# Kernel tuning notes

Measured on AMD Instinct MI355X. Metric: run time of the kernel, lower is better.

## Reference

```python
import jax, jax.numpy as jnp
import numpy as np

B, S, D = 2, 2048, 4096
H, KV, HD = 32, 8, 128          # query heads, kv heads, head_dim
N_REP = H // KV                 # GQA groups = 4
ROPE_THETA = 1000000.0


def setup_inputs() -> dict:
    key = jax.random.key(0)
    ks = jax.random.split(key, 8)
    s = 0.02
    return {
        "hidden_states": jax.random.normal(ks[0], (B, S, D), jnp.float32),
        "position_ids": jnp.broadcast_to(jnp.arange(S, dtype=jnp.int32)[None, :], (B, S)),
        "wq": jax.random.normal(ks[1], (D, H * HD), jnp.float32) * s,
        "bq": jax.random.normal(ks[2], (H * HD,), jnp.float32) * s,
        "wk": jax.random.normal(ks[3], (D, KV * HD), jnp.float32) * s,
        "bk": jax.random.normal(ks[4], (KV * HD,), jnp.float32) * s,
        "wv": jax.random.normal(ks[5], (D, KV * HD), jnp.float32) * s,
        "bv": jax.random.normal(ks[6], (KV * HD,), jnp.float32) * s,
        "wo": jax.random.normal(ks[7], (H * HD, D), jnp.float32) * s,
    }


def _rope_cos_sin(position_ids, head_dim, theta):
    pos = position_ids.astype(jnp.float32)
    dim = head_dim // 2
    freqs = 1.0 / theta ** (jnp.arange(0, dim, dtype=jnp.float32) / dim)
    t = pos[..., None] * freqs[None, None, :]          # [B,S,dim]
    return jnp.cos(t)[..., None, :], jnp.sin(t)[..., None, :]  # [B,S,1,dim]


def _apply_rope(x, cos, sin):
    half = x.shape[-1] // 2
    x1, x2 = x[..., :half], x[..., half:]
    return jnp.concatenate([x1 * cos - x2 * sin, x1 * sin + x2 * cos], axis=-1)


def reference(hidden_states, position_ids, wq, bq, wk, bk, wv, bv, wo):
    q = (hidden_states @ wq + bq).reshape(B, S, H, HD)
    k = (hidden_states @ wk + bk).reshape(B, S, KV, HD)
    v = (hidden_states @ wv + bv).reshape(B, S, KV, HD)

    cos, sin = _rope_cos_sin(position_ids, HD, ROPE_THETA)
    q = _apply_rope(q, cos, sin)
    k = _apply_rope(k, cos, sin)

    # GQA: physically expand KV heads (adjacent repeats, matches repeat_kv)
    k = jnp.repeat(k, N_REP, axis=2)   # [B,S,H,HD]
    v = jnp.repeat(v, N_REP, axis=2)

    # causal bias (attention_mask defaults to all-ones, so only causal matters)
    neg = jnp.finfo(jnp.float32).min
    causal = jnp.tril(jnp.ones((S, S), dtype=bool))
    bias = jnp.where(causal, 0.0, neg).astype(jnp.float32)  # [S,S]

    scale = 1.0 / jnp.sqrt(jnp.float32(HD))
    scores = jnp.einsum("bqhd,bkhd->bhqk", q * scale, k) + bias[None, None]
    attn = jax.nn.softmax(scores, axis=-1)                  # [B,H,S,S]
    out = jnp.einsum("bhqk,bkhd->bqhd", attn, v)
    out = out.reshape(B, S, H * HD)
    return out @ wo
```

## Files before the change

kernel.cpp:

```cpp
#include <hip/hip_runtime.h>
#include <hip/hip_bf16.h>
#include <math.h>


typedef __bf16 bf16;
typedef __attribute__((ext_vector_type(8))) __bf16 bf16x8;
typedef __attribute__((ext_vector_type(4))) float f32x4;

__device__ __forceinline__ void glds16(const void* g, void* l) {
    __builtin_amdgcn_global_load_lds(
        (const __attribute__((address_space(1))) void*)g,
        (__attribute__((address_space(3))) void*)l, 16, 0, 0);
}

__device__ __forceinline__ unsigned cvt_pk_bf16(float lo, float hi) {
    unsigned r;
    asm("v_cvt_pk_bf16_f32 %0, %1, %2" : "=v"(r) : "v"(lo), "v"(hi));
    return r;
}

__global__ __launch_bounds__(256) void convert_kernel(
    const float* __restrict__ in, bf16* __restrict__ out)
{
    const size_t i0 = ((size_t)blockIdx.x * 256 + threadIdx.x) * 8;
    const float4 a = *(const float4*)(in + i0);
    const float4 b = *(const float4*)(in + i0 + 4);
    bf16x8 p;
    p[0] = (bf16)a.x; p[1] = (bf16)a.y; p[2] = (bf16)a.z; p[3] = (bf16)a.w;
    p[4] = (bf16)b.x; p[5] = (bf16)b.y; p[6] = (bf16)b.z; p[7] = (bf16)b.w;
    *(bf16x8*)(out + i0) = p;
}

__global__ __launch_bounds__(256) void transpose_conv_kernel(
    const float* __restrict__ in, bf16* __restrict__ out, int N)
{
    __shared__ bf16 tile[32 * 68];
    const int n0 = blockIdx.x * 32, k0 = blockIdx.y * 64;
    const int t = threadIdx.x;
    const int nn = t & 31, kk0 = (t >> 5) * 8;
#pragma unroll
    for (int j = 0; j < 8; ++j)
        tile[nn * 68 + kk0 + j] = (bf16)in[(size_t)(k0 + kk0 + j) * N + n0 + nn];
    __syncthreads();
    const int n2 = t >> 3, c = (t & 7) * 8;
    *(bf16x8*)(out + (size_t)(n0 + n2) * 4096 + k0 + c) = *(const bf16x8*)(&tile[n2 * 68 + c]);
}

#define G256_LDA(dst, bufv, mh)                                                 \
    do {                                                                        \
        _Pragma("unroll")                                                       \
        for (int m_ = 0; m_ < 4; ++m_) {                                        \
            const int rowh_ = (m_ * 2 + wr) * 16 + l15;                         \
            const int colp_ = (quad * 8) ^ (((rowh_ >> 3) & 1) << 4);           \
            const int bse_ = ((bufv) * 2 + (mh)) * 8192 + rowh_ * 32 + colp_;   \
            dst[m_][0] = *(const bf16x8*)&Lds[bse_];                            \
            dst[m_][1] = *(const bf16x8*)&Lds[bse_ + 4096];                     \
        }                                                                       \
    } while (0)

#define G256_LDB(dst, bufv, nh)                                                 \
    do {                                                                        \
        _Pragma("unroll")                                                       \
        for (int n_ = 0; n_ < 2; ++n_) {                                        \
            const int rowh_ = (n_ * 4 + wc) * 16 + l15;                         \
            const int colp_ = (quad * 8) ^ (((rowh_ >> 3) & 1) << 4);           \
            const int bse_ = 32768 + ((bufv) * 2 + (nh)) * 8192 +               \
                             rowh_ * 32 + colp_;                                \
            dst[n_][0] = *(const bf16x8*)&Lds[bse_];                            \
            dst[n_][1] = *(const bf16x8*)&Lds[bse_ + 4096];                     \
        }                                                                       \
    } while (0)

#define G256_QUAD(av, bv, mh, nh)                                               \
    do {                                                                        \
        __builtin_amdgcn_s_setprio(1);                                          \
        _Pragma("unroll")                                                       \
        for (int m_ = 0; m_ < 4; ++m_)                                          \
            _Pragma("unroll")                                                   \
            for (int n_ = 0; n_ < 2; ++n_) {                                    \
                acc[(mh) * 4 + m_][(nh) * 2 + n_] =                             \
                    __builtin_amdgcn_mfma_f32_16x16x32_bf16(                    \
                        av[m_][0], bv[n_][0], acc[(mh) * 4 + m_][(nh) * 2 + n_],\
                        0, 0, 0);                                               \
                acc[(mh) * 4 + m_][(nh) * 2 + n_] =                             \
                    __builtin_amdgcn_mfma_f32_16x16x32_bf16(                    \
                        av[m_][1], bv[n_][1], acc[(mh) * 4 + m_][(nh) * 2 + n_],\
                        0, 0, 0);                                               \
            }                                                                   \
        __builtin_amdgcn_s_setprio(0);                                          \
    } while (0)

template <int EPI>
__global__ __launch_bounds__(512) void gemm256_kernel(
    const bf16* __restrict__ A,
    const bf16* __restrict__ BqT, const bf16* __restrict__ BkT, const bf16* __restrict__ BvT,
    const float* __restrict__ b_q, const float* __restrict__ b_k, const float* __restrict__ b_v,
    bf16* __restrict__ q_out, bf16* __restrict__ kv_k, bf16* __restrict__ kv_v,
    float* __restrict__ f_out, int nwg)
{
    __shared__ bf16 Lds[65536];

    const int tid = threadIdx.x;
    const int wv = tid >> 6, lane = tid & 63;
    const int l15 = lane & 15, quad = lane >> 4;
    const int wr = wv >> 2, wc = wv & 3;

    const int bid = blockIdx.x;
    const int swz = (bid & 7) * (nwg >> 3) + (bid >> 3);
    const int mt = swz & 15, nt = swz >> 4;
    const int row0 = mt * 256;

    const bf16* BT;
    const float* biasp = nullptr;
    bf16* dstkv = nullptr;
    int sel = 0, bcol0, ocol0 = nt * 256, lcol0 = 0;
    if (EPI == 0) {
        if (nt < 16)      { BT = BqT; bcol0 = nt * 256; biasp = b_q + nt * 256; sel = 0; }
        else if (nt < 20) { BT = BkT; bcol0 = (nt - 16) * 256; biasp = b_k + (nt - 16) * 256;
                            sel = 1; dstkv = kv_k; lcol0 = (nt - 16) * 256; }
        else              { BT = BvT; bcol0 = (nt - 20) * 256; biasp = b_v + (nt - 20) * 256;
                            sel = 2; dstkv = kv_v; lcol0 = (nt - 20) * 256; }
    } else {
        BT = BqT; bcol0 = nt * 256;
    }

    auto stage = [&](int n) {
        if (n >= 256) return;
        const int T = n >> 2, j = n & 3;
        const int buf = T & 1;
        const bool isA = (j == 0 || j == 3);
        const int half = (j == 0) ? 0 : (j == 3) ? 1 : (j - 1);
        const int k0 = T * 64;
        const bf16* g = isA ? (A + (size_t)(row0 + half * 128) * 4096)
                            : (BT + (size_t)(bcol0 + half * 128) * 4096);
        bf16* lb = &Lds[(isA ? 0 : 32768) + (buf * 2 + half) * 8192];
#pragma unroll
        for (int jj = 0; jj < 2; ++jj) {
            const int pc = (wv * 2 + jj) * 64 + lane;
            const int kk = pc >> 9, rem = pc & 511;
            const int row = rem >> 2, ccp = rem & 3;
            const int ccl = ccp ^ ((row >> 2) & 2);
            glds16(g + (size_t)row * 4096 + k0 + kk * 32 + ccl * 8,
                   lb + (wv * 2 + jj) * 512);
        }
    };

    const f32x4 vzero = {0.f, 0.f, 0.f, 0.f};
    f32x4 acc[8][4];
#pragma unroll
    for (int mi = 0; mi < 8; ++mi)
#pragma unroll
        for (int ni = 0; ni < 4; ++ni) acc[mi][ni] = vzero;

    bf16x8 a[4][2], b0[2][2], b1[2][2];

    for (int n = 0; n < 7; ++n) stage(n);
    asm volatile("s_waitcnt vmcnt(6)" ::: "memory");
    __builtin_amdgcn_s_barrier();

    for (int t = 0; t < 64; ++t) {
        const int buf = t & 1;
        const int nb = 4 * t;
        G256_LDA(a, buf, 0);
        G256_LDB(b0, buf, 0);
        stage(nb + 7);
        __builtin_amdgcn_s_barrier();
        G256_QUAD(a, b0, 0, 0);
        __builtin_amdgcn_s_barrier();
        G256_LDB(b1, buf, 1);
        stage(nb + 8);
        __builtin_amdgcn_s_barrier();
        G256_QUAD(a, b1, 0, 1);
        __builtin_amdgcn_s_barrier();
        G256_LDA(a, buf, 1);
        stage(nb + 9);
        __builtin_amdgcn_s_barrier();
        G256_QUAD(a, b0, 1, 0);
        __builtin_amdgcn_s_barrier();
        stage(nb + 10);
        __builtin_amdgcn_s_barrier();
        G256_QUAD(a, b1, 1, 1);
        if (t < 62)       asm volatile("s_waitcnt vmcnt(6)" ::: "memory");
        else if (t == 62) asm volatile("s_waitcnt vmcnt(0)" ::: "memory");
        __builtin_amdgcn_s_barrier();
    }

#pragma unroll
    for (int mi = 0; mi < 8; ++mi) {
        const int mtile = (mi >> 2) * 8 + (mi & 3) * 2 + wr;
#pragma unroll
        for (int ni = 0; ni < 4; ++ni) {
            const int ntile = ni * 4 + wc;
            const int gcl = ntile * 16 + l15;
#pragma unroll
            for (int i = 0; i < 4; ++i) {
                const int gr = row0 + mtile * 16 + quad * 4 + i;
                float vv = acc[mi][ni][i];
                if (EPI == 1) {
                    f_out[(size_t)gr * 4096 + ocol0 + gcl] = vv;
                } else {
                    vv += biasp[gcl];
                    if (sel == 0) {
                        q_out[(size_t)gr * 4096 + ocol0 + gcl] = (bf16)vv;
                    } else {
                        const int lc = lcol0 + gcl;
                        dstkv[(size_t)((gr >> 11) * 8 + (lc >> 7)) * 262144 +
                              (size_t)(gr & 2047) * 128 + (lc & 127)] = (bf16)vv;
                    }
                }
            }
        }
    }
}

template <int EPI, int AF32>
__global__ __launch_bounds__(256) void gemm_kernel(
    const float* __restrict__ A_f32, const bf16* __restrict__ A_bf16,
    const bf16* __restrict__ BqT, const bf16* __restrict__ BkT, const bf16* __restrict__ BvT,
    const float* __restrict__ b_q, const float* __restrict__ b_k, const float* __restrict__ b_v,
    bf16* __restrict__ q_out, bf16* __restrict__ kv_k, bf16* __restrict__ kv_v,
    float* __restrict__ f_out)
{
    constexpr int LDA = AF32 ? 34 : 32;
    __shared__ bf16 As[128 * LDA];
    __shared__ bf16 Bs[128 * 32];

    const int nt = blockIdx.x, mt = blockIdx.y;
    const int tid = threadIdx.x;
    const int wave = tid >> 6, lane = tid & 63;
    const int l15 = lane & 15, quad = lane >> 4;
    const int wm = (wave >> 1) * 64, wn = (wave & 1) * 64;

    const bf16* BT;
    const float* bias = nullptr;
    int sel = 0, ncol0;
    if (EPI == 0) {
        if (nt < 32)      { BT = BqT; bias = b_q; sel = 0; ncol0 = nt * 128; }
        else if (nt < 40) { BT = BkT; bias = b_k; sel = 1; ncol0 = (nt - 32) * 128; }
        else              { BT = BvT; bias = b_v; sel = 2; ncol0 = (nt - 40) * 128; }
    } else {
        BT = BqT; ncol0 = nt * 128;
    }
    const int row0 = mt * 128;

    const f32x4 vzero = {0.f, 0.f, 0.f, 0.f};
    f32x4 acc[4][4];
#pragma unroll
    for (int mi = 0; mi < 4; ++mi)
#pragma unroll
        for (int ni = 0; ni < 4; ++ni) acc[mi][ni] = vzero;

    const int a_row = tid >> 1, a_seg = (tid & 1) * 16;
    const int g_row = lane >> 2, g_seg = (lane & 3) * 8;

    for (int k0 = 0; k0 < 4096; k0 += 32) {
        if (AF32) {
            const float4* src = (const float4*)(A_f32 + (size_t)(row0 + a_row) * 4096 + k0 + a_seg);
            float4 f0 = src[0], f1 = src[1], f2 = src[2], f3 = src[3];
            bf16x8 p0, p1;
            p0[0] = (bf16)f0.x; p0[1] = (bf16)f0.y; p0[2] = (bf16)f0.z; p0[3] = (bf16)f0.w;
            p0[4] = (bf16)f1.x; p0[5] = (bf16)f1.y; p0[6] = (bf16)f1.z; p0[7] = (bf16)f1.w;
            p1[0] = (bf16)f2.x; p1[1] = (bf16)f2.y; p1[2] = (bf16)f2.z; p1[3] = (bf16)f2.w;
            p1[4] = (bf16)f3.x; p1[5] = (bf16)f3.y; p1[6] = (bf16)f3.z; p1[7] = (bf16)f3.w;
            *(bf16x8*)(&As[a_row * LDA + a_seg]) = p0;
            *(bf16x8*)(&As[a_row * LDA + a_seg + 8]) = p1;
        } else {
#pragma unroll
            for (int c = 0; c < 2; ++c)
                glds16(A_bf16 + (size_t)(row0 + wave * 32 + c * 16 + g_row) * 4096 + k0 + g_seg,
                       &As[(wave * 32 + c * 16) * 32]);
        }
#pragma unroll
        for (int c = 0; c < 2; ++c)
            glds16(BT + (size_t)(ncol0 + wave * 32 + c * 16 + g_row) * 4096 + k0 + g_seg,
                   &Bs[(wave * 32 + c * 16) * 32]);
        __syncthreads();

        bf16x8 af[4], bfv[4];
#pragma unroll
        for (int mi = 0; mi < 4; ++mi)
            af[mi] = *(const bf16x8*)(&As[(wm + mi * 16 + l15) * LDA + quad * 8]);
#pragma unroll
        for (int ni = 0; ni < 4; ++ni)
            bfv[ni] = *(const bf16x8*)(&Bs[(wn + ni * 16 + l15) * 32 + quad * 8]);
#pragma unroll
        for (int mi = 0; mi < 4; ++mi)
#pragma unroll
            for (int ni = 0; ni < 4; ++ni)
                acc[mi][ni] = __builtin_amdgcn_mfma_f32_16x16x32_bf16(af[mi], bfv[ni], acc[mi][ni], 0, 0, 0);
        __syncthreads();
    }

#pragma unroll
    for (int mi = 0; mi < 4; ++mi)
#pragma unroll
        for (int ni = 0; ni < 4; ++ni)
#pragma unroll
            for (int i = 0; i < 4; ++i) {
                const int gr = row0 + wm + mi * 16 + quad * 4 + i;
                const int gc = ncol0 + wn + ni * 16 + l15;
                float vv = acc[mi][ni][i];
                if (EPI == 1) {
                    f_out[(size_t)gr * 4096 + gc] = vv;
                } else {
                    vv += bias[gc];
                    if (sel == 0) {
                        q_out[(size_t)gr * 4096 + gc] = (bf16)vv;
                    } else {
                        bf16* dst = (sel == 1) ? kv_k : kv_v;
                        dst[(size_t)((gr >> 11) * 8 + (gc >> 7)) * 262144 +
                            (size_t)(gr & 2047) * 128 + (gc & 127)] = (bf16)vv;
                    }
                }
            }
}

__global__ __launch_bounds__(256) void rope_q_kernel(
    bf16* __restrict__ q, const int* __restrict__ pos_ids)
{
    const int idx = blockIdx.x * 256 + threadIdx.x;
    const int d = idx & 63, h = (idx >> 6) & 31, tok = idx >> 11;
    const float posv = (float)pos_ids[tok];
    const float fr = exp2f((float)d * (-19.931568569324174f / 64.f));
    float sn, cs;
    sincosf(posv * fr, &sn, &cs);
    bf16* xp = q + (size_t)tok * 4096 + h * 128 + d;
    const float x1 = (float)xp[0], x2 = (float)xp[64];
    const float scale = 0.08838834764831845f;
    xp[0]  = (bf16)((x1 * cs - x2 * sn) * scale);
    xp[64] = (bf16)((x1 * sn + x2 * cs) * scale);
}

__global__ __launch_bounds__(256) void rope_k_kernel(
    bf16* __restrict__ k, const int* __restrict__ pos_ids)
{
    const int idx = blockIdx.x * 256 + threadIdx.x;
    const int d = idx & 63, s = (idx >> 6) & 2047, bk = idx >> 17;
    const int b = bk >> 3;
    const float posv = (float)pos_ids[b * 2048 + s];
    const float fr = exp2f((float)d * (-19.931568569324174f / 64.f));
    float sn, cs;
    sincosf(posv * fr, &sn, &cs);
    bf16* xp = k + ((size_t)bk * 2048 + s) * 128 + d;
    const float x1 = (float)xp[0], x2 = (float)xp[64];
    xp[0]  = (bf16)(x1 * cs - x2 * sn);
    xp[64] = (bf16)(x1 * sn + x2 * cs);
}

__global__ __launch_bounds__(256) void attn_kernel(
    const bf16* __restrict__ q, const bf16* __restrict__ k,
    const bf16* __restrict__ v, bf16* __restrict__ o)
{
    __shared__ bf16 Ksl[64 * 136];
    __shared__ bf16 Vsl[128 * 72];
    __shared__ bf16 Psl[4 * 16 * 68];

    const int pair = blockIdx.x & 7;
    const int h  = (blockIdx.x >> 3) & 31;
    const int b  = blockIdx.x >> 8;
    const int kvh = h >> 2;
    const int tid = threadIdx.x;
    const int wave = tid >> 6, lane = tid & 63;
    const int l15 = lane & 15, quad = lane >> 4;

    const bf16* kbase = k + (size_t)(b * 8 + kvh) * 2048 * 128;
    const bf16* vbase = v + (size_t)(b * 8 + kvh) * 2048 * 128;

    const int kr = tid >> 2, ksg = (tid & 3) * 32;
    const f32x4 vzero = {0.f, 0.f, 0.f, 0.f};

#pragma unroll 1
    for (int phase = 0; phase < 2; ++phase) {
        const int qt = phase ? (15 - pair) : pair;
        const int qbase = qt * 128 + wave * 32;

        bf16x8 qf[2][4];
#pragma unroll
        for (int mi = 0; mi < 2; ++mi) {
            const bf16* qrow = q + ((size_t)(b * 2048 + qbase + mi * 16 + l15) * 32 + h) * 128;
#pragma unroll
            for (int kb = 0; kb < 4; ++kb)
                qf[mi][kb] = *(const bf16x8*)(qrow + kb * 32 + quad * 8);
        }

        f32x4 acc_o[2][8];
#pragma unroll
        for (int mi = 0; mi < 2; ++mi)
#pragma unroll
            for (int i = 0; i < 8; ++i) acc_o[mi][i] = vzero;
        float m_i[2] = {-INFINITY, -INFINITY};
        float l_i[2] = {0.f, 0.f};

        const int nT = 2 * qt + 2;
        for (int t = 0; t < nT; ++t) {
            const int kv0 = t * 64;
            {
                const bf16x8* ks = (const bf16x8*)(kbase + (size_t)(kv0 + kr) * 128 + ksg);
                bf16x8* kd = (bf16x8*)(&Ksl[kr * 136 + ksg]);
                kd[0] = ks[0]; kd[1] = ks[1]; kd[2] = ks[2]; kd[3] = ks[3];
            }
            {
                const bf16x8* vs = (const bf16x8*)(vbase + (size_t)(kv0 + lane) * 128 + wave * 32);
                bf16x8 w0 = vs[0], w1 = vs[1], w2 = vs[2], w3 = vs[3];
#pragma unroll
                for (int i = 0; i < 8; ++i) {
                    Vsl[(wave * 32 + i)      * 72 + lane] = w0[i];
                    Vsl[(wave * 32 + 8 + i)  * 72 + lane] = w1[i];
                    Vsl[(wave * 32 + 16 + i) * 72 + lane] = w2[i];
                    Vsl[(wave * 32 + 24 + i) * 72 + lane] = w3[i];
                }
            }
            __syncthreads();

            if (kv0 <= qbase + 31) {
                f32x4 sacc[2][4];
#pragma unroll
                for (int mi = 0; mi < 2; ++mi)
#pragma unroll
                    for (int nt = 0; nt < 4; ++nt) sacc[mi][nt] = vzero;
                __builtin_amdgcn_s_setprio(1);
#pragma unroll
                for (int nt = 0; nt < 4; ++nt)
#pragma unroll
                    for (int kb = 0; kb < 4; ++kb) {
                        const bf16x8 kf = *(const bf16x8*)(&Ksl[(nt * 16 + l15) * 136 + kb * 32 + quad * 8]);
                        sacc[0][nt] = __builtin_amdgcn_mfma_f32_16x16x32_bf16(kf, qf[0][kb], sacc[0][nt], 0, 0, 0);
                        sacc[1][nt] = __builtin_amdgcn_mfma_f32_16x16x32_bf16(kf, qf[1][kb], sacc[1][nt], 0, 0, 0);
                    }
                __builtin_amdgcn_s_setprio(0);

                bf16x8 pf[2][2];
#pragma unroll
                for (int mi = 0; mi < 2; ++mi) {
                    const int rb = qbase + mi * 16;
                    if (kv0 + 63 > rb) {
#pragma unroll
                        for (int nt = 0; nt < 4; ++nt) {
                            const int kvr = kv0 + nt * 16 + quad * 4;
#pragma unroll
                            for (int i = 0; i < 4; ++i)
                                if (kvr + i > rb + l15) sacc[mi][nt][i] = -INFINITY;
                        }
                    }
                    float tm;
                    {
                        f32x4 m4;
#pragma unroll
                        for (int i = 0; i < 4; ++i)
                            m4[i] = fmaxf(fmaxf(sacc[mi][0][i], sacc[mi][1][i]),
                                          fmaxf(sacc[mi][2][i], sacc[mi][3][i]));
                        tm = fmaxf(fmaxf(m4[0], m4[1]), fmaxf(m4[2], m4[3]));
                        tm = fmaxf(tm, __shfl_xor(tm, 16, 64));
                        tm = fmaxf(tm, __shfl_xor(tm, 32, 64));
                    }
                    if (!__all(tm - m_i[mi] <= 8.f)) {
                        const float mnew = fmaxf(m_i[mi], tm);
                        const float alpha = __expf(m_i[mi] - mnew);
                        m_i[mi] = mnew;
                        l_i[mi] *= alpha;
                        float aw[4];
#pragma unroll
                        for (int i = 0; i < 4; ++i)
                            aw[i] = __shfl(alpha, quad * 4 + i, 16);
#pragma unroll
                        for (int dn = 0; dn < 8; ++dn)
#pragma unroll
                            for (int i = 0; i < 4; ++i) acc_o[mi][dn][i] *= aw[i];
                    }
                    float p[4][4];
                    float rs = 0.f;
#pragma unroll
                    for (int nt = 0; nt < 4; ++nt)
#pragma unroll
                        for (int i = 0; i < 4; ++i) {
                            p[nt][i] = __expf(sacc[mi][nt][i] - m_i[mi]);
                            rs += p[nt][i];
                        }
                    rs += __shfl_xor(rs, 16, 64);
                    rs += __shfl_xor(rs, 32, 64);
                    l_i[mi] += rs;
#pragma unroll
                    for (int nt = 0; nt < 4; ++nt) {
                        uint2 w;
                        w.x = cvt_pk_bf16(p[nt][0], p[nt][1]);
                        w.y = cvt_pk_bf16(p[nt][2], p[nt][3]);
                        *(uint2*)(&Psl[wave * 1088 + l15 * 68 + nt * 16 + quad * 4]) = w;
                    }
#pragma unroll
                    for (int k2 = 0; k2 < 2; ++k2)
                        pf[mi][k2] = *(const bf16x8*)(&Psl[wave * 1088 + l15 * 68 + k2 * 32 + quad * 8]);
                }

                __builtin_amdgcn_s_setprio(1);
#pragma unroll
                for (int dn = 0; dn < 8; ++dn)
#pragma unroll
                    for (int k2 = 0; k2 < 2; ++k2) {
                        const bf16x8 vf = *(const bf16x8*)(&Vsl[(dn * 16 + l15) * 72 + k2 * 32 + quad * 8]);
                        acc_o[0][dn] = __builtin_amdgcn_mfma_f32_16x16x32_bf16(pf[0][k2], vf, acc_o[0][dn], 0, 0, 0);
                        acc_o[1][dn] = __builtin_amdgcn_mfma_f32_16x16x32_bf16(pf[1][k2], vf, acc_o[1][dn], 0, 0, 0);
                    }
                __builtin_amdgcn_s_setprio(0);
            }
            __syncthreads();
        }

#pragma unroll
        for (int mi = 0; mi < 2; ++mi) {
            const float inv = 1.f / l_i[mi];
            float invw[4];
#pragma unroll
            for (int i = 0; i < 4; ++i)
                invw[i] = __shfl(inv, quad * 4 + i, 16);
#pragma unroll
            for (int dn = 0; dn < 8; ++dn)
#pragma unroll
                for (int i = 0; i < 4; ++i) {
                    const int s = qbase + mi * 16 + quad * 4 + i;
                    o[(((size_t)b * 2048 + s) * 32 + h) * 128 + dn * 16 + l15] =
                        (bf16)(acc_o[mi][dn][i] * invw[i]);
                }
        }
    }
}

extern "C" void kernel_launch(void* const* d_in, const int* in_sizes, int n_in,
                              void* d_out, int out_size, void* d_ws, size_t ws_size,
                              hipStream_t stream)
{
    (void)in_sizes; (void)n_in; (void)out_size;
    const float* hidden = (const float*)d_in[0];
    const int*   pos    = (const int*)d_in[1];
    const float* wq     = (const float*)d_in[2];
    const float* bq_    = (const float*)d_in[3];
    const float* wk     = (const float*)d_in[4];
    const float* bk_    = (const float*)d_in[5];
    const float* wv     = (const float*)d_in[6];
    const float* bv_    = (const float*)d_in[7];
    const float* wo     = (const float*)d_in[8];
    float* out = (float*)d_out;

    char* ws = (char*)d_ws;
    bf16* wqT   = (bf16*)(ws);
    bf16* wkT   = (bf16*)(ws + 33554432);
    bf16* wvT   = (bf16*)(ws + 41943040);
    bf16* q_pre = (bf16*)(ws + 50331648);
    bf16* k_t   = (bf16*)(ws + 83886080);
    bf16* v_t   = (bf16*)(ws + 92274688);
    bf16* hid_b = (bf16*)(ws + 100663296);
    bf16* attn_o = wqT;
    bf16* woT    = q_pre;
    const bool have_hid = (ws_size >= 134217728);

    transpose_conv_kernel<<<dim3(128, 64), 256, 0, stream>>>(wq, wqT, 4096);
    transpose_conv_kernel<<<dim3(32, 64), 256, 0, stream>>>(wk, wkT, 1024);
    transpose_conv_kernel<<<dim3(32, 64), 256, 0, stream>>>(wv, wvT, 1024);

    if (have_hid) {
        convert_kernel<<<8192, 256, 0, stream>>>(hidden, hid_b);
        gemm256_kernel<0><<<384, 512, 0, stream>>>(
            hid_b, wqT, wkT, wvT, bq_, bk_, bv_, q_pre, k_t, v_t, nullptr, 384);
    } else {
        gemm_kernel<0, 1><<<dim3(48, 32), 256, 0, stream>>>(
            hidden, nullptr, wqT, wkT, wvT, bq_, bk_, bv_, q_pre, k_t, v_t, nullptr);
    }

    rope_q_kernel<<<32768, 256, 0, stream>>>(q_pre, pos);
    rope_k_kernel<<<8192, 256, 0, stream>>>(k_t, pos);

    attn_kernel<<<512, 256, 0, stream>>>(q_pre, k_t, v_t, attn_o);

    transpose_conv_kernel<<<dim3(128, 64), 256, 0, stream>>>(wo, woT, 4096);

    if (have_hid) {
        gemm256_kernel<1><<<256, 512, 0, stream>>>(
            attn_o, woT, nullptr, nullptr, nullptr, nullptr, nullptr,
            nullptr, nullptr, nullptr, out, 256);
    } else {
        gemm_kernel<1, 0><<<dim3(32, 32), 256, 0, stream>>>(
            nullptr, attn_o, woT, nullptr, nullptr, nullptr, nullptr, nullptr,
            nullptr, nullptr, nullptr, out);
    }
}
```

Baseline: 796.7 us.

## Replace QKV projection GEMM with 128x256-tile kernel using 768 blocks

Adds a dedicated QKV projection GEMM that uses 128x256 output tiles, for 768 workgroups instead of 384 with 256x256 tiles. It uses a BK=64 double-buffered global-to-LDS pipeline with XOR-swizzled LDS, split B halves interleaved with MFMA phases, and an XCD-aware block swizzle. The aim is better load balance and occupancy across CUs for the 4096x6144x4096 projection. The trade-off is lower per-tile arithmetic intensity and more global traffic for A.

```diff
diff --git a/kernel.cpp b/kernel.cpp
--- a/kernel.cpp
+++ b/kernel.cpp
@@ -44,6 +44,133 @@
     __syncthreads();
     const int n2 = t >> 3, c = (t & 7) * 8;
     *(bf16x8*)(out + (size_t)(n0 + n2) * 4096 + k0 + c) = *(const bf16x8*)(&tile[n2 * 68 + c]);
+}
+
+#define QKV_LDA(dst, bufv)                                                    \
+  { _Pragma("unroll") for (int m_ = 0; m_ < 4; ++m_) {                        \
+      const int row_ = (wr * 4 + m_) * 16 + l15;                              \
+      const int bse_ = (bufv) * 8192 + row_ * 64;                             \
+      dst[m_][0] = *(const bf16x8*)&Lds[bse_ + ((quad * 8) ^ xk)];            \
+      dst[m_][1] = *(const bf16x8*)&Lds[bse_ + ((32 + quad * 8) ^ xk)];       \
+    } }
+
+#define QKV_LDB(dst, bufv, nh)                                                \
+  { _Pragma("unroll") for (int n_ = 0; n_ < 2; ++n_) {                        \
+      const int rowh_ = (n_ * 4 + wc) * 16 + l15;                             \
+      const int bse_ = 16384 + ((bufv) * 2 + (nh)) * 8192 + rowh_ * 64;       \
+      dst[n_][0] = *(const bf16x8*)&Lds[bse_ + ((quad * 8) ^ xk)];            \
+      dst[n_][1] = *(const bf16x8*)&Lds[bse_ + ((32 + quad * 8) ^ xk)];       \
+    } }
+
+#define QKV_QUAD(av, bv, nh)                                                  \
+  { __builtin_amdgcn_s_setprio(1);                                           \
+    _Pragma("unroll") for (int m_ = 0; m_ < 4; ++m_)                          \
+      _Pragma("unroll") for (int n_ = 0; n_ < 2; ++n_) {                      \
+        acc[m_][(nh) * 2 + n_] = __builtin_amdgcn_mfma_f32_16x16x32_bf16(     \
+            av[m_][0], bv[n_][0], acc[m_][(nh) * 2 + n_], 0, 0, 0);           \
+        acc[m_][(nh) * 2 + n_] = __builtin_amdgcn_mfma_f32_16x16x32_bf16(     \
+            av[m_][1], bv[n_][1], acc[m_][(nh) * 2 + n_], 0, 0, 0);           \
+      }                                                                       \
+    __builtin_amdgcn_s_setprio(0); }
+
+__global__ __launch_bounds__(512) void gemm_qkv_kernel(
+    const bf16* __restrict__ A,
+    const bf16* __restrict__ BqT, const bf16* __restrict__ BkT, const bf16* __restrict__ BvT,
+    const float* __restrict__ b_q, const float* __restrict__ b_k, const float* __restrict__ b_v,
+    bf16* __restrict__ q_out, bf16* __restrict__ kv_k, bf16* __restrict__ kv_v)
+{
+    __shared__ bf16 Lds[49152];
+
+    const int tid = threadIdx.x;
+    const int wv = tid >> 6, lane = tid & 63;
+    const int l15 = lane & 15, quad = lane >> 4;
+    const int wr = wv >> 2, wc = wv & 3;
+    const int xk = (l15 & 7) * 8;
+
+    const int bid = blockIdx.x;
+    const int swz = (bid & 7) * 96 + (bid >> 3);
+    const int mt = swz / 24, nt = swz % 24;
+    const int row0 = mt * 128;
+
+    const bf16* BT;
+    const float* biasp;
+    bf16* dstkv = nullptr;
+    int sel, bcol0, lcol0 = 0, qcol0 = 0;
+    if (nt < 16)      { BT = BqT; bcol0 = nt * 256; biasp = b_q + bcol0; sel = 0; qcol0 = bcol0; }
+    else if (nt < 20) { BT = BkT; bcol0 = (nt - 16) * 256; biasp = b_k + bcol0; sel = 1;
+                        dstkv = kv_k; lcol0 = bcol0; }
+    else              { BT = BvT; bcol0 = (nt - 20) * 256; biasp = b_v + bcol0; sel = 2;
+                        dstkv = kv_v; lcol0 = bcol0; }
+
+    auto stage = [&](int T, int j) {
+        if (T >= 64) return;
+        const int buf = T & 1;
+        const int k0 = T * 64;
+        const int r = wv * 8 + (lane >> 3);
+        const int gcol = k0 + (((lane & 7) * 8) ^ ((r & 7) * 8));
+        const bf16* g;
+        int ldsbase;
+        if (j < 2) {
+            g = A + (size_t)(row0 + j * 64 + r) * 4096 + gcol;
+            ldsbase = buf * 8192 + j * 4096;
+        } else {
+            const int half = (j - 2) >> 1, sub = (j - 2) & 1;
+            g = BT + (size_t)(bcol0 + half * 128 + sub * 64 + r) * 4096 + gcol;
+            ldsbase = 16384 + (buf * 2 + half) * 8192 + sub * 4096;
+        }
+        glds16(g, &Lds[ldsbase + wv * 512]);
+    };
+
+    const f32x4 vzero = {0.f, 0.f, 0.f, 0.f};
+    f32x4 acc[4][4];
+#pragma unroll
+    for (int m_ = 0; m_ < 4; ++m_)
+#pragma unroll
+        for (int n_ = 0; n_ < 4; ++n_) acc[m_][n_] = vzero;
+
+    bf16x8 a[4][2], b0[2][2], b1[2][2];
+
+    for (int j = 0; j < 6; ++j) stage(0, j);
+    for (int j = 0; j < 4; ++j) stage(1, j);
+    asm volatile("s_waitcnt vmcnt(4)" ::: "memory");
+    __builtin_amdgcn_s_barrier();
+
+    for (int t = 0; t < 64; ++t) {
+        const int buf = t & 1;
+        QKV_LDA(a, buf);
+        QKV_LDB(b0, buf, 0);
+        stage(t + 1, 4); stage(t + 1, 5);
+        __builtin_amdgcn_s_barrier();
+        QKV_QUAD(a, b0, 0);
+        __builtin_amdgcn_s_barrier();
+        QKV_LDB(b1, buf, 1);
+        stage(t + 2, 0); stage(t + 2, 1); stage(t + 2, 2); stage(t + 2, 3);
+        __builtin_amdgcn_s_barrier();
+        QKV_QUAD(a, b1, 1);
+        if (t < 62)       asm volatile("s_waitcnt vmcnt(4)" ::: "memory");
+        else if (t == 62) asm volatile("s_waitcnt vmcnt(0)" ::: "memory");
+        __builtin_amdgcn_s_barrier();
+    }
+
+#pragma unroll
+    for (int m_ = 0; m_ < 4; ++m_) {
+#pragma unroll
+        for (int n_ = 0; n_ < 4; ++n_) {
+            const int gcl = (n_ * 4 + wc) * 16 + l15;
+#pragma unroll
+            for (int i = 0; i < 4; ++i) {
+                const int gr = row0 + (wr * 4 + m_) * 16 + quad * 4 + i;
+                float vv = acc[m_][n_][i] + biasp[gcl];
+                if (sel == 0) {
+                    q_out[(size_t)gr * 4096 + qcol0 + gcl] = (bf16)vv;
+                } else {
+                    const int lc = lcol0 + gcl;
+                    dstkv[(size_t)((gr >> 11) * 8 + (lc >> 7)) * 262144 +
+                          (size_t)(gr & 2047) * 128 + (lc & 127)] = (bf16)vv;
+                }
+            }
+        }
+    }
 }
 
 #define G256_LDA(dst, bufv, mh)                                                 \
@@ -558,8 +685,8 @@
 
     if (have_hid) {
         convert_kernel<<<8192, 256, 0, stream>>>(hidden, hid_b);
-        gemm256_kernel<0><<<384, 512, 0, stream>>>(
-            hid_b, wqT, wkT, wvT, bq_, bk_, bv_, q_pre, k_t, v_t, nullptr, 384);
+        gemm_qkv_kernel<<<768, 512, 0, stream>>>(
+            hid_b, wqT, wkT, wvT, bq_, bk_, bv_, q_pre, k_t, v_t);
     } else {
         gemm_kernel<0, 1><<<dim3(48, 32), 256, 0, stream>>>(
             hidden, nullptr, wqT, wkT, wvT, bq_, bk_, bv_, q_pre, k_t, v_t, nullptr);
```

Measured after the change: 789.4 us. No clear change (-0.9%).
